# Optimization experiments

Measured on AMD Instinct MI355X. Metric: run time of the kernel, lower is better.

## Reference

```python
import jax, jax.numpy as jnp
import numpy as np

N = 50000
E = 800000
IN = 128
H = 128
C = 64
BN_EPS = 1e-5


def gcn_conv(x, W, b, src, dst, n_nodes):
    # GCNConv: add self-loops, symmetric normalization D^-1/2 (A+I) D^-1/2, linear, bias
    deg = jax.ops.segment_sum(jnp.ones_like(dst, dtype=x.dtype), dst, num_segments=n_nodes)
    dinv = jnp.where(deg > 0, jax.lax.rsqrt(deg), jnp.zeros_like(deg))
    norm = dinv[src] * dinv[dst]                      # [E+N]
    h = x @ W                                         # [N, out]
    agg = jax.ops.segment_sum(norm[:, None] * h[src], dst, num_segments=n_nodes)
    return agg + b


def batch_norm_eval(x, gamma, beta, mean, var):
    return gamma * (x - mean) * jax.lax.rsqrt(var + BN_EPS) + beta


def setup_inputs() -> dict:
    key = jax.random.key(0)
    ks = jax.random.split(key, 16)
    inp = {
        "x": jax.random.normal(ks[0], (N, IN), dtype=jnp.float32),
        "edge_index": jax.random.randint(ks[1], (2, E), 0, N, dtype=jnp.int64),
        "W1": jax.random.normal(ks[2], (IN, H), dtype=jnp.float32) / np.sqrt(IN),
        "b1": jnp.zeros((H,), dtype=jnp.float32),
        "g1": jnp.ones((H,), dtype=jnp.float32),
        "be1": jnp.zeros((H,), dtype=jnp.float32),
        "m1": jax.random.normal(ks[3], (H,), dtype=jnp.float32) * 0.1,
        "v1": jax.random.uniform(ks[4], (H,), dtype=jnp.float32, minval=0.5, maxval=1.5),
        "W2": jax.random.normal(ks[5], (H, H), dtype=jnp.float32) / np.sqrt(H),
        "b2": jnp.zeros((H,), dtype=jnp.float32),
        "g2": jnp.ones((H,), dtype=jnp.float32),
        "be2": jnp.zeros((H,), dtype=jnp.float32),
        "m2": jax.random.normal(ks[6], (H,), dtype=jnp.float32) * 0.1,
        "v2": jax.random.uniform(ks[7], (H,), dtype=jnp.float32, minval=0.5, maxval=1.5),
        "W3": jax.random.normal(ks[8], (H, C), dtype=jnp.float32) / np.sqrt(H),
        "b3": jnp.zeros((C,), dtype=jnp.float32),
    }
    return inp


def reference(x, edge_index, W1, b1, g1, be1, m1, v1, W2, b2, g2, be2, m2, v2, W3, b3):
    # add self loops once (shared across layers, GCNConv cached=True)
    loop = jnp.arange(N, dtype=edge_index.dtype)
    src = jnp.concatenate([edge_index[0], loop])
    dst = jnp.concatenate([edge_index[1], loop])

    h = gcn_conv(x, W1, b1, src, dst, N)
    h = jax.nn.relu(batch_norm_eval(h, g1, be1, m1, v1))  # eval mode: dropout is identity
    h = gcn_conv(h, W2, b2, src, dst, N)
    h = jax.nn.relu(batch_norm_eval(h, g2, be2, m2, v2))
    out = gcn_conv(h, W3, b3, src, dst, N)
    return out
```

## Files before the change

### kernel.cpp

```cpp
#include <hip/hip_runtime.h>


#define SCAN_CHUNK 1024
#define NCHUNK 256
#define BSHIFT 8
#define BWID 256
#define ECAP 8192

typedef __attribute__((ext_vector_type(8))) short bf16x8;
typedef __attribute__((ext_vector_type(4))) float f32x4;

__device__ __forceinline__ float blo(unsigned p) { return __uint_as_float(p << 16); }
__device__ __forceinline__ float bhi(unsigned p) { return __uint_as_float(p & 0xffff0000u); }
__device__ __forceinline__ unsigned short f2b(float f) {
  unsigned u = __float_as_uint(f);
  unsigned r = (u + 0x7fffu + ((u >> 16) & 1u)) >> 16;
  return (unsigned short)r;
}

__global__ void wprep_kernel(const float* __restrict__ W1, const float* __restrict__ W2,
                             const float* __restrict__ W3,
                             const float* __restrict__ b1, const float* __restrict__ g1,
                             const float* __restrict__ be1, const float* __restrict__ m1,
                             const float* __restrict__ v1,
                             const float* __restrict__ b2, const float* __restrict__ g2,
                             const float* __restrict__ be2, const float* __restrict__ m2,
                             const float* __restrict__ v2,
                             unsigned short* __restrict__ Wt1,
                             unsigned short* __restrict__ Wt2,
                             unsigned short* __restrict__ Wt3,
                             float* __restrict__ sc1, float* __restrict__ sh1,
                             float* __restrict__ sc2, float* __restrict__ sh2) {
  int i = blockIdx.x * 256 + threadIdx.x;
  if (i < 16384) {
    int k = i >> 7, c = i & 127;
    Wt1[c * 128 + k] = f2b(W1[i]);
  } else if (i < 32768) {
    int j = i - 16384; int k = j >> 7, c = j & 127;
    Wt2[c * 128 + k] = f2b(W2[j]);
  } else if (i < 40960) {
    int j = i - 32768; int k = j >> 6, c = j & 63;
    Wt3[c * 128 + k] = f2b(W3[j]);
  } else if (i < 41088) {
    int c = i - 40960;
    float s = g1[c] * rsqrtf(v1[c] + 1e-5f);
    sc1[c] = s; sh1[c] = (b1[c] - m1[c]) * s + be1[c];
  } else if (i < 41216) {
    int c = i - 41088;
    float s = g2[c] * rsqrtf(v2[c] + 1e-5f);
    sc2[c] = s; sh2[c] = (b2[c] - m2[c]) * s + be2[c];
  }
}

__global__ __launch_bounds__(256) void bin_hist_kernel(
    const int* __restrict__ ei32, const long long* __restrict__ ei64,
    int* __restrict__ counts, int E, int nbk) {
  __shared__ int hist[BWID];
  __shared__ int s_is32;
  int k = blockIdx.x, t = threadIdx.x;
  hist[t] = 0;
  if (t == 0) s_is32 = 0;
  int CH = (E + NCHUNK - 1) / NCHUNK;
  int e0 = k * CH, e1 = min(e0 + CH, E);
  __syncthreads();
  if (t < 64 && e0 + t < E && ei32[2 * (e0 + t) + 1] != 0) atomicOr(&s_is32, 1);
  __syncthreads();
  int is32 = s_is32;
  for (int e = e0 + t; e < e1; e += 256) {
    int d = is32 ? ei32[E + e] : (int)ei64[E + e];
    atomicAdd(&hist[d >> BSHIFT], 1);
  }
  __syncthreads();
  if (t < nbk) counts[t * NCHUNK + k] = hist[t];
}

__global__ __launch_bounds__(256) void scan_partial_kernel(
    const int* __restrict__ src, int* __restrict__ bsum, int n) {
  __shared__ int wsum[4];
  int b = blockIdx.x, t = threadIdx.x;
  int lane = t & 63, wv = t >> 6;
  int i0 = b * SCAN_CHUNK + t * 4;
  int4 d4 = make_int4(0, 0, 0, 0);
  if (i0 + 3 < n) d4 = *(const int4*)&src[i0];
  else {
    if (i0 < n) d4.x = src[i0];
    if (i0 + 1 < n) d4.y = src[i0 + 1];
    if (i0 + 2 < n) d4.z = src[i0 + 2];
  }
  int s = d4.x + d4.y + d4.z + d4.w;
#pragma unroll
  for (int off = 32; off; off >>= 1) s += __shfl_xor(s, off);
  if (lane == 0) wsum[wv] = s;
  __syncthreads();
  if (t == 0) bsum[b] = wsum[0] + wsum[1] + wsum[2] + wsum[3];
}

template <bool DEG>
__global__ __launch_bounds__(256) void scan_write_kernel(
    const int* __restrict__ src, const int* __restrict__ bsum,
    int* __restrict__ outp, float* __restrict__ dinv, int n, int nb) {
  __shared__ int woff[4];
  __shared__ int s_boff;
  int b = blockIdx.x, t = threadIdx.x;
  int lane = t & 63, wv = t >> 6;
  if (t < 64) {
    int v = (t < nb) ? bsum[t] : 0;
    int ic = v;
#pragma unroll
    for (int off = 1; off < 64; off <<= 1) {
      int u = __shfl_up(ic, off);
      if (t >= off) ic += u;
    }
    if (t == b) s_boff = ic - v;
    if (b == nb - 1 && t == 63) outp[n] = ic;
  }
  int i0 = b * SCAN_CHUNK + t * 4;
  int4 d4 = make_int4(0, 0, 0, 0);
  if (i0 + 3 < n) d4 = *(const int4*)&src[i0];
  else {
    if (i0 < n) d4.x = src[i0];
    if (i0 + 1 < n) d4.y = src[i0 + 1];
    if (i0 + 2 < n) d4.z = src[i0 + 2];
  }
  int tsum = d4.x + d4.y + d4.z + d4.w;
  int inc = tsum;
#pragma unroll
  for (int off = 1; off < 64; off <<= 1) {
    int u = __shfl_up(inc, off);
    if (lane >= off) inc += u;
  }
  if (lane == 63) woff[wv] = inc;
  __syncthreads();
  if (t == 0) {
    int r = 0;
#pragma unroll
    for (int w = 0; w < 4; ++w) { int sw = woff[w]; woff[w] = r; r += sw; }
  }
  __syncthreads();
  int p = inc - tsum + woff[wv] + s_boff;
  int dg[4] = {d4.x, d4.y, d4.z, d4.w};
#pragma unroll
  for (int j = 0; j < 4; ++j) {
    int i = i0 + j;
    if (i < n) {
      outp[i] = p;
      if constexpr (DEG) dinv[i] = rsqrtf((float)(dg[j] + 1));
      p += dg[j];
    }
  }
}

__global__ __launch_bounds__(256) void bin_scatter_kernel(
    const int* __restrict__ ei32, const long long* __restrict__ ei64,
    const int* __restrict__ offs, unsigned* __restrict__ pairs, int E, int nbk) {
  __shared__ int cur[BWID];
  __shared__ int s_is32;
  int k = blockIdx.x, t = threadIdx.x;
  if (t < nbk) cur[t] = offs[t * NCHUNK + k];
  if (t == 0) s_is32 = 0;
  int CH = (E + NCHUNK - 1) / NCHUNK;
  int e0 = k * CH, e1 = min(e0 + CH, E);
  __syncthreads();
  if (t < 64 && e0 + t < E && ei32[2 * (e0 + t) + 1] != 0) atomicOr(&s_is32, 1);
  __syncthreads();
  int is32 = s_is32;
  for (int e = e0 + t; e < e1; e += 256) {
    int s, d;
    if (is32) { s = ei32[e]; d = ei32[E + e]; }
    else      { s = (int)ei64[e]; d = (int)ei64[E + e]; }
    int pos = atomicAdd(&cur[d >> BSHIFT], 1);
    pairs[pos] = (unsigned)s | ((unsigned)(d & (BWID - 1)) << 20);
  }
}

__global__ __launch_bounds__(256) void bucket_deg_kernel(
    const unsigned* __restrict__ pairs, const int* __restrict__ offs,
    int* __restrict__ degi, int E, int n, int nbk) {
  __shared__ int deg[BWID];
  int b = blockIdx.x, t = threadIdx.x;
  deg[t] = 0;
  __syncthreads();
  int base = offs[b * NCHUNK];
  int end = (b + 1 < nbk) ? offs[(b + 1) * NCHUNK] : E;
  for (int i = base + t; i < end; i += 256) {
    atomicAdd(&deg[pairs[i] >> 20], 1);
  }
  __syncthreads();
  int idx = b * BWID + t;
  if (idx < n) degi[idx] = deg[t];
}

__global__ __launch_bounds__(256) void bucket_col_kernel(
    const unsigned* __restrict__ pairs, const int* __restrict__ offs,
    const int* __restrict__ rowptr, const float* __restrict__ dinv,
    uint2* __restrict__ cw, int E, int n, int nbk) {
  __shared__ int cur[BWID];
  __shared__ float dsl[BWID];
  __shared__ int stage_s[ECAP];
  __shared__ float stage_w[ECAP];
  int b = blockIdx.x, t = threadIdx.x;
  int rowbase = rowptr[b * BWID];
  int idx = b * BWID + t;
  cur[t] = ((idx < n) ? rowptr[idx] : rowptr[n]) - rowbase;
  dsl[t] = (idx < n) ? dinv[idx] : 0.f;
  __syncthreads();
  int base = offs[b * NCHUNK];
  int end = (b + 1 < nbk) ? offs[(b + 1) * NCHUNK] : E;
  for (int i = base + t; i < end; i += 256) {
    unsigned p = pairs[i];
    int s = (int)(p & 0xFFFFFu);
    int dl = (int)(p >> 20);
    int pos = atomicAdd(&cur[dl], 1);
    if (pos < ECAP) { stage_s[pos] = s; stage_w[pos] = dinv[s] * dsl[dl]; }
  }
  __syncthreads();
  int hi = b * BWID + BWID;
  int nE = ((hi < n) ? rowptr[hi] : rowptr[n]) - rowbase;
  for (int i = t; i < nE; i += 256)
    cw[rowbase + i] = make_uint2((unsigned)stage_s[i], __float_as_uint(stage_w[i]));
}

template <int HOUT, int ABF16>
__global__ __launch_bounds__(256) void mgemm_kernel(
    const void* __restrict__ Ain, const unsigned short* __restrict__ Wt,
    unsigned short* __restrict__ Y, int n) {
  constexpr int NT = HOUT;
  __shared__ unsigned char AsB[64 * 256];
  __shared__ unsigned char BsB[NT * 256];
  int t = threadIdx.x;
  int row0 = blockIdx.x * 64;

  if constexpr (ABF16) {
    const unsigned short* A = (const unsigned short*)Ain;
#pragma unroll
    for (int jj = 0; jj < 4; ++jj) {
      int f = t + 256 * jj; int r = f >> 4, kq = f & 15;
      uint4 v = make_uint4(0, 0, 0, 0);
      if (row0 + r < n) v = *(const uint4*)&A[(size_t)(row0 + r) * 128 + kq * 8];
      *(uint4*)&AsB[r * 256 + ((kq * 16) ^ ((r & 15) << 4))] = v;
    }
  } else {
    const float* A = (const float*)Ain;
#pragma unroll
    for (int jj = 0; jj < 8; ++jj) {
      int f = t + 256 * jj; int r = f >> 5, kq = f & 31;
      float4 v = make_float4(0.f, 0.f, 0.f, 0.f);
      if (row0 + r < n) v = *(const float4*)&A[(size_t)(row0 + r) * 128 + kq * 4];
      unsigned two0 = (unsigned)f2b(v.x) | ((unsigned)f2b(v.y) << 16);
      unsigned two1 = (unsigned)f2b(v.z) | ((unsigned)f2b(v.w) << 16);
      uint2 o = make_uint2(two0, two1);
      *(uint2*)&AsB[r * 256 + ((kq * 8) ^ ((r & 15) << 4))] = o;
    }
  }
#pragma unroll
  for (int jj = 0; jj < NT / 16; ++jj) {
    int f = t + 256 * jj; int c = f >> 4, kq = f & 15;
    uint4 v = *(const uint4*)&Wt[(size_t)c * 128 + kq * 8];
    *(uint4*)&BsB[c * 256 + ((kq * 16) ^ ((c & 15) << 4))] = v;
  }
  __syncthreads();

  int l = t & 63, wid = t >> 6;
  constexpr int WC = NT / 2;
  constexpr int NI = WC / 16;
  int wr = (wid >> 1) * 32, wc = (wid & 1) * WC;
  int lr = l & 15, lk = (l >> 4) * 16;

  f32x4 acc[2][NI] = {};
#pragma unroll
  for (int ks = 0; ks < 4; ++ks) {
    bf16x8 a[2], b[NI];
#pragma unroll
    for (int mi = 0; mi < 2; ++mi) {
      int r = wr + mi * 16 + lr;
      a[mi] = *(const bf16x8*)&AsB[r * 256 + ((ks * 64 + lk) ^ ((r & 15) << 4))];
    }
#pragma unroll
    for (int ni = 0; ni < NI; ++ni) {
      int c = wc + ni * 16 + lr;
      b[ni] = *(const bf16x8*)&BsB[c * 256 + ((ks * 64 + lk) ^ ((c & 15) << 4))];
    }
#pragma unroll
    for (int mi = 0; mi < 2; ++mi)
#pragma unroll
      for (int ni = 0; ni < NI; ++ni)
        acc[mi][ni] = __builtin_amdgcn_mfma_f32_16x16x32_bf16(a[mi], b[ni],
                                                              acc[mi][ni], 0, 0, 0);
  }

#pragma unroll
  for (int mi = 0; mi < 2; ++mi) {
#pragma unroll
    for (int reg = 0; reg < 4; ++reg) {
      int gr = row0 + wr + mi * 16 + (l >> 4) * 4 + reg;
      if (gr < n) {
#pragma unroll
        for (int ni = 0; ni < NI; ++ni) {
          int gc = wc + ni * 16 + lr;
          Y[(size_t)gr * HOUT + gc] = f2b(acc[mi][ni][reg]);
        }
      }
    }
  }
}

template <int HOUT, bool BN, bool OUTBF>
__global__ __launch_bounds__(256) void agg_kernel(
    const unsigned short* __restrict__ h, const int* __restrict__ rowptr,
    const uint2* __restrict__ cw, const float* __restrict__ dinv,
    const float* __restrict__ sc, const float* __restrict__ sh,
    void* __restrict__ out, int n_nodes) {
  int n = (blockIdx.x * blockDim.x + threadIdx.x) >> 6;
  if (n >= n_nodes) return;
  int lane = threadIdx.x & 63;
  const uint2* hu2 = (const uint2*)h;
  constexpr int RW2 = HOUT / 4;
  constexpr int NPH = (HOUT == 128) ? 2 : 4;
  constexpr int GL = 64 / NPH;
  int phase = lane / GL;
  int sub = lane & (GL - 1);

  float dn = dinv[n];
  int beg = rowptr[n], end = rowptr[n + 1];
  float a0 = 0.f, a1 = 0.f, a2 = 0.f, a3 = 0.f;
  if (phase == 0) {
    uint2 sp = hu2[(size_t)n * RW2 + sub];
    float sw = dn * dn;
    a0 = sw * blo(sp.x); a1 = sw * bhi(sp.x);
    a2 = sw * blo(sp.y); a3 = sw * bhi(sp.y);
  }

  int j = beg + phase;
  for (; j + 3 * NPH < end; j += 4 * NPH) {
    uint2 e0 = cw[j], e1 = cw[j + NPH], e2 = cw[j + 2 * NPH], e3 = cw[j + 3 * NPH];
    uint2 h0 = hu2[(size_t)e0.x * RW2 + sub];
    uint2 h1 = hu2[(size_t)e1.x * RW2 + sub];
    uint2 h2 = hu2[(size_t)e2.x * RW2 + sub];
    uint2 h3 = hu2[(size_t)e3.x * RW2 + sub];
    float w0 = __uint_as_float(e0.y), w1 = __uint_as_float(e1.y);
    float w2 = __uint_as_float(e2.y), w3 = __uint_as_float(e3.y);
    a0 = fmaf(w0, blo(h0.x), a0); a1 = fmaf(w0, bhi(h0.x), a1);
    a2 = fmaf(w0, blo(h0.y), a2); a3 = fmaf(w0, bhi(h0.y), a3);
    a0 = fmaf(w1, blo(h1.x), a0); a1 = fmaf(w1, bhi(h1.x), a1);
    a2 = fmaf(w1, blo(h1.y), a2); a3 = fmaf(w1, bhi(h1.y), a3);
    a0 = fmaf(w2, blo(h2.x), a0); a1 = fmaf(w2, bhi(h2.x), a1);
    a2 = fmaf(w2, blo(h2.y), a2); a3 = fmaf(w2, bhi(h2.y), a3);
    a0 = fmaf(w3, blo(h3.x), a0); a1 = fmaf(w3, bhi(h3.x), a1);
    a2 = fmaf(w3, blo(h3.y), a2); a3 = fmaf(w3, bhi(h3.y), a3);
  }
  for (; j < end; j += NPH) {
    uint2 e = cw[j];
    uint2 hv = hu2[(size_t)e.x * RW2 + sub];
    float w = __uint_as_float(e.y);
    a0 = fmaf(w, blo(hv.x), a0); a1 = fmaf(w, bhi(hv.x), a1);
    a2 = fmaf(w, blo(hv.y), a2); a3 = fmaf(w, bhi(hv.y), a3);
  }

  a0 += __shfl_xor(a0, 32); a1 += __shfl_xor(a1, 32);
  a2 += __shfl_xor(a2, 32); a3 += __shfl_xor(a3, 32);
  if constexpr (NPH == 4) {
    a0 += __shfl_xor(a0, 16); a1 += __shfl_xor(a1, 16);
    a2 += __shfl_xor(a2, 16); a3 += __shfl_xor(a3, 16);
  }
  if (phase != 0) return;

  int c0 = sub * 4;
  float y0, y1, y2, y3;
  if constexpr (BN) {
    y0 = fmaxf(fmaf(a0, sc[c0], sh[c0]), 0.f);
    y1 = fmaxf(fmaf(a1, sc[c0 + 1], sh[c0 + 1]), 0.f);
    y2 = fmaxf(fmaf(a2, sc[c0 + 2], sh[c0 + 2]), 0.f);
    y3 = fmaxf(fmaf(a3, sc[c0 + 3], sh[c0 + 3]), 0.f);
  } else {
    y0 = a0 + sh[c0]; y1 = a1 + sh[c0 + 1];
    y2 = a2 + sh[c0 + 2]; y3 = a3 + sh[c0 + 3];
  }
  if constexpr (OUTBF) {
    unsigned p0 = (unsigned)f2b(y0) | ((unsigned)f2b(y1) << 16);
    unsigned p1 = (unsigned)f2b(y2) | ((unsigned)f2b(y3) << 16);
    ((uint2*)out)[(size_t)n * RW2 + sub] = make_uint2(p0, p1);
  } else {
    float4 o; o.x = y0; o.y = y1; o.z = y2; o.w = y3;
    *(float4*)&((float*)out)[(size_t)n * HOUT + c0] = o;
  }
}

extern "C" void kernel_launch(void* const* d_in, const int* in_sizes, int n_in,
                              void* d_out, int out_size, void* d_ws, size_t ws_size,
                              hipStream_t stream) {
  const float* x = (const float*)d_in[0];
  const int* ei32 = (const int*)d_in[1];
  const long long* ei64 = (const long long*)d_in[1];
  const float* W1 = (const float*)d_in[2];
  const float* b1 = (const float*)d_in[3];
  const float* g1 = (const float*)d_in[4];
  const float* be1 = (const float*)d_in[5];
  const float* m1 = (const float*)d_in[6];
  const float* v1 = (const float*)d_in[7];
  const float* W2 = (const float*)d_in[8];
  const float* b2 = (const float*)d_in[9];
  const float* g2 = (const float*)d_in[10];
  const float* be2 = (const float*)d_in[11];
  const float* m2 = (const float*)d_in[12];
  const float* v2 = (const float*)d_in[13];
  const float* W3 = (const float*)d_in[14];
  const float* b3 = (const float*)d_in[15];

  const int N = in_sizes[0] / 128;
  const int E = in_sizes[1] / 2;
  const int NBK = (N + BWID - 1) / BWID;
  const int NC = NBK * NCHUNK;

  char* ws = (char*)d_ws;
  size_t off = 0;
  auto alloc = [&](size_t bytes) -> void* {
    void* p = ws + off;
    off = (off + bytes + 255) & ~(size_t)255;
    return p;
  };
  float* dinv = (float*)alloc((size_t)N * 4);
  int* rowptr = (int*)alloc((size_t)(N + 1) * 4);
  int* degi = (int*)alloc((size_t)N * 4);
  int* counts = (int*)alloc((size_t)(NC + 1) * 4);
  int* offs = (int*)alloc((size_t)(NC + 1) * 4);
  uint2* cw = (uint2*)alloc((size_t)E * 8);
  unsigned* pairs = (unsigned*)alloc((size_t)E * 4);
  int* bsum = (int*)alloc(64 * 4);
  unsigned short* wt1 = (unsigned short*)alloc(128 * 128 * 2);
  unsigned short* wt2 = (unsigned short*)alloc(128 * 128 * 2);
  unsigned short* wt3 = (unsigned short*)alloc(128 * 64 * 2);
  float* sc1 = (float*)alloc(128 * 4);
  float* sh1 = (float*)alloc(128 * 4);
  float* sc2 = (float*)alloc(128 * 4);
  float* sh2 = (float*)alloc(128 * 4);
  unsigned short* hbuf = (unsigned short*)alloc((size_t)N * 128 * 2);
  unsigned short* ybuf = (unsigned short*)alloc((size_t)N * 128 * 2);
  (void)ws_size;

  wprep_kernel<<<161, 256, 0, stream>>>(W1, W2, W3, b1, g1, be1, m1, v1,
                                        b2, g2, be2, m2, v2,
                                        wt1, wt2, wt3, sc1, sh1, sc2, sh2);

  bin_hist_kernel<<<NCHUNK, 256, 0, stream>>>(ei32, ei64, counts, E, NBK);
  int nbC = (NC + SCAN_CHUNK - 1) / SCAN_CHUNK;
  scan_partial_kernel<<<nbC, 256, 0, stream>>>(counts, bsum, NC);
  scan_write_kernel<false><<<nbC, 256, 0, stream>>>(counts, bsum, offs, nullptr, NC, nbC);
  bin_scatter_kernel<<<NCHUNK, 256, 0, stream>>>(ei32, ei64, offs, pairs, E, NBK);
  bucket_deg_kernel<<<NBK, 256, 0, stream>>>(pairs, offs, degi, E, N, NBK);
  int nbN = (N + SCAN_CHUNK - 1) / SCAN_CHUNK;
  scan_partial_kernel<<<nbN, 256, 0, stream>>>(degi, bsum, N);
  scan_write_kernel<true><<<nbN, 256, 0, stream>>>(degi, bsum, rowptr, dinv, N, nbN);
  bucket_col_kernel<<<NBK, 256, 0, stream>>>(pairs, offs, rowptr, dinv, cw, E, N, NBK);

  int gb = (N + 63) / 64;
  int ab = (N + 3) / 4;

  mgemm_kernel<128, 0><<<gb, 256, 0, stream>>>(x, wt1, hbuf, N);
  agg_kernel<128, true, true><<<ab, 256, 0, stream>>>(hbuf, rowptr, cw, dinv,
                                                      sc1, sh1, ybuf, N);
  mgemm_kernel<128, 1><<<gb, 256, 0, stream>>>(ybuf, wt2, hbuf, N);
  agg_kernel<128, true, true><<<ab, 256, 0, stream>>>(hbuf, rowptr, cw, dinv,
                                                      sc2, sh2, ybuf, N);
  mgemm_kernel<64, 1><<<gb, 256, 0, stream>>>(ybuf, wt3, hbuf, N);
  agg_kernel<64, false, false><<<ab, 256, 0, stream>>>(hbuf, rowptr, cw, dinv,
                                                       nullptr, b3, d_out, N);
}
```

Baseline: 188.7 us.

## Sort edges by source slab, fold self-loops into CSR, widen aggregation loads

The binning key now combines the destination bucket with a source slab of 8192 nodes. Edges inside each row are then roughly ordered by source, which should improve cache locality of the gathers during aggregation. The degree pass computes rowptr and dinv directly from per-bucket offsets plus self-loops, which removes the separate node-level scan kernels. Self-loops are written as explicit CSR entries, so the aggregation kernel no longer handles them specially. That kernel now loads 16-byte bf16 vectors with more edges per phase. In exchange the count array is 8 times larger, there is an overflow path for rows beyond the staging capacity, and register use per lane is higher.

```diff
diff --git a/kernel.cpp b/kernel.cpp
--- a/kernel.cpp
+++ b/kernel.cpp
@@ -1,10 +1,11 @@
 #include <hip/hip_runtime.h>
 
 
-#define SCAN_CHUNK 1024
 #define NCHUNK 256
 #define BSHIFT 8
 #define BWID 256
+#define NSLAB 8
+#define SSHIFT 13
 #define ECAP 8192
 
 typedef __attribute__((ext_vector_type(8))) short bf16x8;
@@ -54,11 +55,11 @@
 
 __global__ __launch_bounds__(256) void bin_hist_kernel(
     const int* __restrict__ ei32, const long long* __restrict__ ei64,
-    int* __restrict__ counts, int E, int nbk) {
-  __shared__ int hist[BWID];
+    int* __restrict__ counts, int E, int nkeys) {
+  __shared__ int hist[2048];
   __shared__ int s_is32;
   int k = blockIdx.x, t = threadIdx.x;
-  hist[t] = 0;
+  for (int i = t; i < nkeys; i += 256) hist[i] = 0;
   if (t == 0) s_is32 = 0;
   int CH = (E + NCHUNK - 1) / NCHUNK;
   int e0 = k * CH, e1 = min(e0 + CH, E);
@@ -67,27 +68,34 @@
   __syncthreads();
   int is32 = s_is32;
   for (int e = e0 + t; e < e1; e += 256) {
-    int d = is32 ? ei32[E + e] : (int)ei64[E + e];
-    atomicAdd(&hist[d >> BSHIFT], 1);
-  }
-  __syncthreads();
-  if (t < nbk) counts[t * NCHUNK + k] = hist[t];
-}
-
+    int s, d;
+    if (is32) { s = ei32[e]; d = ei32[E + e]; }
+    else      { s = (int)ei64[e]; d = (int)ei64[E + e]; }
+    atomicAdd(&hist[((d >> BSHIFT) << 3) | (s >> SSHIFT)], 1);
+  }
+  __syncthreads();
+  for (int i = t; i < nkeys; i += 256) counts[i * NCHUNK + k] = hist[i];
+}
+
+template <int CHUNK>
 __global__ __launch_bounds__(256) void scan_partial_kernel(
     const int* __restrict__ src, int* __restrict__ bsum, int n) {
   __shared__ int wsum[4];
+  constexpr int EL = CHUNK / 256;
   int b = blockIdx.x, t = threadIdx.x;
   int lane = t & 63, wv = t >> 6;
-  int i0 = b * SCAN_CHUNK + t * 4;
-  int4 d4 = make_int4(0, 0, 0, 0);
-  if (i0 + 3 < n) d4 = *(const int4*)&src[i0];
-  else {
-    if (i0 < n) d4.x = src[i0];
-    if (i0 + 1 < n) d4.y = src[i0 + 1];
-    if (i0 + 2 < n) d4.z = src[i0 + 2];
-  }
-  int s = d4.x + d4.y + d4.z + d4.w;
+  int s = 0;
+  int i0 = b * CHUNK + t * EL;
+#pragma unroll
+  for (int q = 0; q < EL / 4; ++q) {
+    int i = i0 + q * 4;
+    if (i + 3 < n) {
+      int4 d4 = *(const int4*)&src[i];
+      s += d4.x + d4.y + d4.z + d4.w;
+    } else {
+      for (int r = 0; r < 4; ++r) if (i + r < n) s += src[i + r];
+    }
+  }
 #pragma unroll
   for (int off = 32; off; off >>= 1) s += __shfl_xor(s, off);
   if (lane == 0) wsum[wv] = s;
@@ -95,10 +103,11 @@
   if (t == 0) bsum[b] = wsum[0] + wsum[1] + wsum[2] + wsum[3];
 }
 
-template <bool DEG>
+template <int CHUNK>
 __global__ __launch_bounds__(256) void scan_write_kernel(
     const int* __restrict__ src, const int* __restrict__ bsum,
-    int* __restrict__ outp, float* __restrict__ dinv, int n, int nb) {
+    int* __restrict__ outp, int n, int nb) {
+  constexpr int EL = CHUNK / 256;
   __shared__ int woff[4];
   __shared__ int s_boff;
   int b = blockIdx.x, t = threadIdx.x;
@@ -114,15 +123,24 @@
     if (t == b) s_boff = ic - v;
     if (b == nb - 1 && t == 63) outp[n] = ic;
   }
-  int i0 = b * SCAN_CHUNK + t * 4;
-  int4 d4 = make_int4(0, 0, 0, 0);
-  if (i0 + 3 < n) d4 = *(const int4*)&src[i0];
-  else {
-    if (i0 < n) d4.x = src[i0];
-    if (i0 + 1 < n) d4.y = src[i0 + 1];
-    if (i0 + 2 < n) d4.z = src[i0 + 2];
-  }
-  int tsum = d4.x + d4.y + d4.z + d4.w;
+  int vals[EL];
+  int i0 = b * CHUNK + t * EL;
+#pragma unroll
+  for (int q = 0; q < EL / 4; ++q) {
+    int i = i0 + q * 4;
+    int4 d4 = make_int4(0, 0, 0, 0);
+    if (i + 3 < n) d4 = *(const int4*)&src[i];
+    else {
+      if (i < n) d4.x = src[i];
+      if (i + 1 < n) d4.y = src[i + 1];
+      if (i + 2 < n) d4.z = src[i + 2];
+    }
+    vals[q * 4] = d4.x; vals[q * 4 + 1] = d4.y;
+    vals[q * 4 + 2] = d4.z; vals[q * 4 + 3] = d4.w;
+  }
+  int tsum = 0;
+#pragma unroll
+  for (int q = 0; q < EL; ++q) tsum += vals[q];
   int inc = tsum;
 #pragma unroll
   for (int off = 1; off < 64; off <<= 1) {
@@ -138,25 +156,21 @@
   }
   __syncthreads();
   int p = inc - tsum + woff[wv] + s_boff;
-  int dg[4] = {d4.x, d4.y, d4.z, d4.w};
-#pragma unroll
-  for (int j = 0; j < 4; ++j) {
-    int i = i0 + j;
-    if (i < n) {
-      outp[i] = p;
-      if constexpr (DEG) dinv[i] = rsqrtf((float)(dg[j] + 1));
-      p += dg[j];
-    }
+#pragma unroll
+  for (int q = 0; q < EL; ++q) {
+    int i = i0 + q;
+    if (i < n) outp[i] = p;
+    p += vals[q];
   }
 }
 
 __global__ __launch_bounds__(256) void bin_scatter_kernel(
     const int* __restrict__ ei32, const long long* __restrict__ ei64,
-    const int* __restrict__ offs, unsigned* __restrict__ pairs, int E, int nbk) {
-  __shared__ int cur[BWID];
+    const int* __restrict__ offs, unsigned* __restrict__ pairs, int E, int nkeys) {
+  __shared__ int cur[2048];
   __shared__ int s_is32;
   int k = blockIdx.x, t = threadIdx.x;
-  if (t < nbk) cur[t] = offs[t * NCHUNK + k];
+  for (int i = t; i < nkeys; i += 256) cur[i] = offs[i * NCHUNK + k];
   if (t == 0) s_is32 = 0;
   int CH = (E + NCHUNK - 1) / NCHUNK;
   int e0 = k * CH, e1 = min(e0 + CH, E);
@@ -168,56 +182,88 @@
     int s, d;
     if (is32) { s = ei32[e]; d = ei32[E + e]; }
     else      { s = (int)ei64[e]; d = (int)ei64[E + e]; }
-    int pos = atomicAdd(&cur[d >> BSHIFT], 1);
+    int pos = atomicAdd(&cur[((d >> BSHIFT) << 3) | (s >> SSHIFT)], 1);
     pairs[pos] = (unsigned)s | ((unsigned)(d & (BWID - 1)) << 20);
   }
 }
 
-__global__ __launch_bounds__(256) void bucket_deg_kernel(
+__global__ __launch_bounds__(256) void bucket_p1_kernel(
     const unsigned* __restrict__ pairs, const int* __restrict__ offs,
-    int* __restrict__ degi, int E, int n, int nbk) {
+    int* __restrict__ rowptr, float* __restrict__ dinv, int E, int n) {
   __shared__ int deg[BWID];
+  __shared__ int woff[4];
   int b = blockIdx.x, t = threadIdx.x;
+  int lane = t & 63, wv = t >> 6;
   deg[t] = 0;
   __syncthreads();
-  int base = offs[b * NCHUNK];
-  int end = (b + 1 < nbk) ? offs[(b + 1) * NCHUNK] : E;
-  for (int i = base + t; i < end; i += 256) {
+  int basep = offs[b * NSLAB * NCHUNK];
+  int endp = offs[(b + 1) * NSLAB * NCHUNK];
+  for (int i = basep + t; i < endp; i += 256)
     atomicAdd(&deg[pairs[i] >> 20], 1);
-  }
-  __syncthreads();
+  __syncthreads();
+  int dg = deg[t];
+  int inc = dg + 1;
+#pragma unroll
+  for (int off = 1; off < 64; off <<= 1) {
+    int u = __shfl_up(inc, off);
+    if (lane >= off) inc += u;
+  }
+  if (lane == 63) woff[wv] = inc;
+  __syncthreads();
+  if (t == 0) {
+    int r = 0;
+#pragma unroll
+    for (int w = 0; w < 4; ++w) { int sw = woff[w]; woff[w] = r; r += sw; }
+  }
+  __syncthreads();
+  int exc = inc - (dg + 1) + woff[wv];
+  int cwbase = basep + b * BWID;
   int idx = b * BWID + t;
-  if (idx < n) degi[idx] = deg[t];
-}
-
-__global__ __launch_bounds__(256) void bucket_col_kernel(
+  if (idx < n) {
+    rowptr[idx] = cwbase + exc;
+    dinv[idx] = rsqrtf((float)(dg + 1));
+  }
+  if (b == 0 && t == 0) rowptr[n] = E + n;
+}
+
+__global__ __launch_bounds__(256) void bucket_p2_kernel(
     const unsigned* __restrict__ pairs, const int* __restrict__ offs,
     const int* __restrict__ rowptr, const float* __restrict__ dinv,
-    uint2* __restrict__ cw, int E, int n, int nbk) {
+    uint2* __restrict__ cw, int E, int n) {
   __shared__ int cur[BWID];
   __shared__ float dsl[BWID];
   __shared__ int stage_s[ECAP];
   __shared__ float stage_w[ECAP];
   int b = blockIdx.x, t = threadIdx.x;
-  int rowbase = rowptr[b * BWID];
+  int basep = offs[b * NSLAB * NCHUNK];
+  int endp = offs[(b + 1) * NSLAB * NCHUNK];
+  int cwbase = basep + b * BWID;
   int idx = b * BWID + t;
-  cur[t] = ((idx < n) ? rowptr[idx] : rowptr[n]) - rowbase;
-  dsl[t] = (idx < n) ? dinv[idx] : 0.f;
-  __syncthreads();
-  int base = offs[b * NCHUNK];
-  int end = (b + 1 < nbk) ? offs[(b + 1) * NCHUNK] : E;
-  for (int i = base + t; i < end; i += 256) {
+  int nreal = min(n - b * BWID, BWID);
+  float dv = (t < nreal) ? dinv[idx] : 0.f;
+  dsl[t] = dv;
+  cur[t] = (t < nreal) ? rowptr[idx] - cwbase : 0;
+  __syncthreads();
+  if (t < nreal) {
+    int pos = atomicAdd(&cur[t], 1);
+    if (pos < ECAP) { stage_s[pos] = idx; stage_w[pos] = dv * dv; }
+    else cw[cwbase + pos] = make_uint2((unsigned)idx, __float_as_uint(dv * dv));
+  }
+  __syncthreads();
+  for (int i = basep + t; i < endp; i += 256) {
     unsigned p = pairs[i];
     int s = (int)(p & 0xFFFFFu);
     int dl = (int)(p >> 20);
     int pos = atomicAdd(&cur[dl], 1);
-    if (pos < ECAP) { stage_s[pos] = s; stage_w[pos] = dinv[s] * dsl[dl]; }
-  }
-  __syncthreads();
-  int hi = b * BWID + BWID;
-  int nE = ((hi < n) ? rowptr[hi] : rowptr[n]) - rowbase;
-  for (int i = t; i < nE; i += 256)
-    cw[rowbase + i] = make_uint2((unsigned)stage_s[i], __float_as_uint(stage_w[i]));
+    float w = dinv[s] * dsl[dl];
+    if (pos < ECAP) { stage_s[pos] = s; stage_w[pos] = w; }
+    else cw[cwbase + pos] = make_uint2((unsigned)s, __float_as_uint(w));
+  }
+  __syncthreads();
+  int nE = (endp - basep) + nreal;
+  int lim = min(nE, ECAP);
+  for (int i = t; i < lim; i += 256)
+    cw[cwbase + i] = make_uint2((unsigned)stage_s[i], __float_as_uint(stage_w[i]));
 }
 
 template <int HOUT, int ABF16>
@@ -307,81 +353,85 @@
 template <int HOUT, bool BN, bool OUTBF>
 __global__ __launch_bounds__(256) void agg_kernel(
     const unsigned short* __restrict__ h, const int* __restrict__ rowptr,
-    const uint2* __restrict__ cw, const float* __restrict__ dinv,
+    const uint2* __restrict__ cw,
     const float* __restrict__ sc, const float* __restrict__ sh,
     void* __restrict__ out, int n_nodes) {
   int n = (blockIdx.x * blockDim.x + threadIdx.x) >> 6;
   if (n >= n_nodes) return;
   int lane = threadIdx.x & 63;
-  const uint2* hu2 = (const uint2*)h;
-  constexpr int RW2 = HOUT / 4;
-  constexpr int NPH = (HOUT == 128) ? 2 : 4;
-  constexpr int GL = 64 / NPH;
+  constexpr int GL = HOUT / 8;
+  constexpr int NPH = 64 / GL;
   int phase = lane / GL;
   int sub = lane & (GL - 1);
-
-  float dn = dinv[n];
+  const uint4* hu = (const uint4*)h;
+
   int beg = rowptr[n], end = rowptr[n + 1];
-  float a0 = 0.f, a1 = 0.f, a2 = 0.f, a3 = 0.f;
-  if (phase == 0) {
-    uint2 sp = hu2[(size_t)n * RW2 + sub];
-    float sw = dn * dn;
-    a0 = sw * blo(sp.x); a1 = sw * bhi(sp.x);
-    a2 = sw * blo(sp.y); a3 = sw * bhi(sp.y);
-  }
+  float a[8] = {0.f, 0.f, 0.f, 0.f, 0.f, 0.f, 0.f, 0.f};
 
   int j = beg + phase;
   for (; j + 3 * NPH < end; j += 4 * NPH) {
     uint2 e0 = cw[j], e1 = cw[j + NPH], e2 = cw[j + 2 * NPH], e3 = cw[j + 3 * NPH];
-    uint2 h0 = hu2[(size_t)e0.x * RW2 + sub];
-    uint2 h1 = hu2[(size_t)e1.x * RW2 + sub];
-    uint2 h2 = hu2[(size_t)e2.x * RW2 + sub];
-    uint2 h3 = hu2[(size_t)e3.x * RW2 + sub];
+    uint4 h0 = hu[(size_t)e0.x * GL + sub];
+    uint4 h1 = hu[(size_t)e1.x * GL + sub];
+    uint4 h2 = hu[(size_t)e2.x * GL + sub];
+    uint4 h3 = hu[(size_t)e3.x * GL + sub];
     float w0 = __uint_as_float(e0.y), w1 = __uint_as_float(e1.y);
     float w2 = __uint_as_float(e2.y), w3 = __uint_as_float(e3.y);
-    a0 = fmaf(w0, blo(h0.x), a0); a1 = fmaf(w0, bhi(h0.x), a1);
-    a2 = fmaf(w0, blo(h0.y), a2); a3 = fmaf(w0, bhi(h0.y), a3);
-    a0 = fmaf(w1, blo(h1.x), a0); a1 = fmaf(w1, bhi(h1.x), a1);
-    a2 = fmaf(w1, blo(h1.y), a2); a3 = fmaf(w1, bhi(h1.y), a3);
-    a0 = fmaf(w2, blo(h2.x), a0); a1 = fmaf(w2, bhi(h2.x), a1);
-    a2 = fmaf(w2, blo(h2.y), a2); a3 = fmaf(w2, bhi(h2.y), a3);
-    a0 = fmaf(w3, blo(h3.x), a0); a1 = fmaf(w3, bhi(h3.x), a1);
-    a2 = fmaf(w3, blo(h3.y), a2); a3 = fmaf(w3, bhi(h3.y), a3);
+    a[0] = fmaf(w0, blo(h0.x), a[0]); a[1] = fmaf(w0, bhi(h0.x), a[1]);
+    a[2] = fmaf(w0, blo(h0.y), a[2]); a[3] = fmaf(w0, bhi(h0.y), a[3]);
+    a[4] = fmaf(w0, blo(h0.z), a[4]); a[5] = fmaf(w0, bhi(h0.z), a[5]);
+    a[6] = fmaf(w0, blo(h0.w), a[6]); a[7] = fmaf(w0, bhi(h0.w), a[7]);
+    a[0] = fmaf(w1, blo(h1.x), a[0]); a[1] = fmaf(w1, bhi(h1.x), a[1]);
+    a[2] = fmaf(w1, blo(h1.y), a[2]); a[3] = fmaf(w1, bhi(h1.y), a[3]);
+    a[4] = fmaf(w1, blo(h1.z), a[4]); a[5] = fmaf(w1, bhi(h1.z), a[5]);
+    a[6] = fmaf(w1, blo(h1.w), a[6]); a[7] = fmaf(w1, bhi(h1.w), a[7]);
+    a[0] = fmaf(w2, blo(h2.x), a[0]); a[1] = fmaf(w2, bhi(h2.x), a[1]);
+    a[2] = fmaf(w2, blo(h2.y), a[2]); a[3] = fmaf(w2, bhi(h2.y), a[3]);
+    a[4] = fmaf(w2, blo(h2.z), a[4]); a[5] = fmaf(w2, bhi(h2.z), a[5]);
+    a[6] = fmaf(w2, blo(h2.w), a[6]); a[7] = fmaf(w2, bhi(h2.w), a[7]);
+    a[0] = fmaf(w3, blo(h3.x), a[0]); a[1] = fmaf(w3, bhi(h3.x), a[1]);
+    a[2] = fmaf(w3, blo(h3.y), a[2]); a[3] = fmaf(w3, bhi(h3.y), a[3]);
+    a[4] = fmaf(w3, blo(h3.z), a[4]); a[5] = fmaf(w3, bhi(h3.z), a[5]);
+    a[6] = fmaf(w3, blo(h3.w), a[6]); a[7] = fmaf(w3, bhi(h3.w), a[7]);
   }
   for (; j < end; j += NPH) {
     uint2 e = cw[j];
-    uint2 hv = hu2[(size_t)e.x * RW2 + sub];
+    uint4 hv = hu[(size_t)e.x * GL + sub];
     float w = __uint_as_float(e.y);
-    a0 = fmaf(w, blo(hv.x), a0); a1 = fmaf(w, bhi(hv.x), a1);
-    a2 = fmaf(w, blo(hv.y), a2); a3 = fmaf(w, bhi(hv.y), a3);
-  }
-
-  a0 += __shfl_xor(a0, 32); a1 += __shfl_xor(a1, 32);
-  a2 += __shfl_xor(a2, 32); a3 += __shfl_xor(a3, 32);
-  if constexpr (NPH == 4) {
-    a0 += __shfl_xor(a0, 16); a1 += __shfl_xor(a1, 16);
-    a2 += __shfl_xor(a2, 16); a3 += __shfl_xor(a3, 16);
+    a[0] = fmaf(w, blo(hv.x), a[0]); a[1] = fmaf(w, bhi(hv.x), a[1]);
+    a[2] = fmaf(w, blo(hv.y), a[2]); a[3] = fmaf(w, bhi(hv.y), a[3]);
+    a[4] = fmaf(w, blo(hv.z), a[4]); a[5] = fmaf(w, bhi(hv.z), a[5]);
+    a[6] = fmaf(w, blo(hv.w), a[6]); a[7] = fmaf(w, bhi(hv.w), a[7]);
+  }
+
+#pragma unroll
+  for (int q = 0; q < 8; ++q) {
+    a[q] += __shfl_xor(a[q], 32);
+    a[q] += __shfl_xor(a[q], 16);
+    if constexpr (NPH == 8) a[q] += __shfl_xor(a[q], 8);
   }
   if (phase != 0) return;
 
-  int c0 = sub * 4;
-  float y0, y1, y2, y3;
-  if constexpr (BN) {
-    y0 = fmaxf(fmaf(a0, sc[c0], sh[c0]), 0.f);
-    y1 = fmaxf(fmaf(a1, sc[c0 + 1], sh[c0 + 1]), 0.f);
-    y2 = fmaxf(fmaf(a2, sc[c0 + 2], sh[c0 + 2]), 0.f);
-    y3 = fmaxf(fmaf(a3, sc[c0 + 3], sh[c0 + 3]), 0.f);
+  int c0 = sub * 8;
+  float y[8];
+#pragma unroll
+  for (int q = 0; q < 8; ++q) {
+    if constexpr (BN) y[q] = fmaxf(fmaf(a[q], sc[c0 + q], sh[c0 + q]), 0.f);
+    else y[q] = a[q] + sh[c0 + q];
+  }
+  if constexpr (OUTBF) {
+    uint4 o;
+    o.x = (unsigned)f2b(y[0]) | ((unsigned)f2b(y[1]) << 16);
+    o.y = (unsigned)f2b(y[2]) | ((unsigned)f2b(y[3]) << 16);
+    o.z = (unsigned)f2b(y[4]) | ((unsigned)f2b(y[5]) << 16);
+    o.w = (unsigned)f2b(y[6]) | ((unsigned)f2b(y[7]) << 16);
+    ((uint4*)out)[(size_t)n * GL + sub] = o;
   } else {
-    y0 = a0 + sh[c0]; y1 = a1 + sh[c0 + 1];
-    y2 = a2 + sh[c0 + 2]; y3 = a3 + sh[c0 + 3];
-  }
-  if constexpr (OUTBF) {
-    unsigned p0 = (unsigned)f2b(y0) | ((unsigned)f2b(y1) << 16);
-    unsigned p1 = (unsigned)f2b(y2) | ((unsigned)f2b(y3) << 16);
-    ((uint2*)out)[(size_t)n * RW2 + sub] = make_uint2(p0, p1);
-  } else {
-    float4 o; o.x = y0; o.y = y1; o.z = y2; o.w = y3;
-    *(float4*)&((float*)out)[(size_t)n * HOUT + c0] = o;
+    float* op = (float*)out + (size_t)n * HOUT + c0;
+    float4 o0; o0.x = y[0]; o0.y = y[1]; o0.z = y[2]; o0.w = y[3];
+    float4 o1; o1.x = y[4]; o1.y = y[5]; o1.z = y[6]; o1.w = y[7];
+    *(float4*)op = o0;
+    *(float4*)(op + 4) = o1;
   }
 }
 
@@ -409,7 +459,8 @@
   const int N = in_sizes[0] / 128;
   const int E = in_sizes[1] / 2;
   const int NBK = (N + BWID - 1) / BWID;
-  const int NC = NBK * NCHUNK;
+  const int NKEYS = NBK * NSLAB;
+  const int NC = NKEYS * NCHUNK;
 
   char* ws = (char*)d_ws;
   size_t off = 0;
@@ -420,11 +471,10 @@
   };
   float* dinv = (float*)alloc((size_t)N * 4);
   int* rowptr = (int*)alloc((size_t)(N + 1) * 4);
-  int* degi = (int*)alloc((size_t)N * 4);
-  int* counts = (int*)alloc((size_t)(NC + 1) * 4);
+  int* counts = (int*)alloc((size_t)NC * 4);
   int* offs = (int*)alloc((size_t)(NC + 1) * 4);
-  uint2* cw = (uint2*)alloc((size_t)E * 8);
   unsigned* pairs = (unsigned*)alloc((size_t)E * 4);
+  uint2* cw = (uint2*)alloc((size_t)(E + N) * 8);
   int* bsum = (int*)alloc(64 * 4);
   unsigned short* wt1 = (unsigned short*)alloc(128 * 128 * 2);
   unsigned short* wt2 = (unsigned short*)alloc(128 * 128 * 2);
@@ -441,27 +491,24 @@
                                         b2, g2, be2, m2, v2,
                                         wt1, wt2, wt3, sc1, sh1, sc2, sh2);
 
-  bin_hist_kernel<<<NCHUNK, 256, 0, stream>>>(ei32, ei64, counts, E, NBK);
-  int nbC = (NC + SCAN_CHUNK - 1) / SCAN_CHUNK;
-  scan_partial_kernel<<<nbC, 256, 0, stream>>>(counts, bsum, NC);
-  scan_write_kernel<false><<<nbC, 256, 0, stream>>>(counts, bsum, offs, nullptr, NC, nbC);
-  bin_scatter_kernel<<<NCHUNK, 256, 0, stream>>>(ei32, ei64, offs, pairs, E, NBK);
-  bucket_deg_kernel<<<NBK, 256, 0, stream>>>(pairs, offs, degi, E, N, NBK);
-  int nbN = (N + SCAN_CHUNK - 1) / SCAN_CHUNK;
-  scan_partial_kernel<<<nbN, 256, 0, stream>>>(degi, bsum, N);
-  scan_write_kernel<true><<<nbN, 256, 0, stream>>>(degi, bsum, rowptr, dinv, N, nbN);
-  bucket_col_kernel<<<NBK, 256, 0, stream>>>(pairs, offs, rowptr, dinv, cw, E, N, NBK);
+  bin_hist_kernel<<<NCHUNK, 256, 0, stream>>>(ei32, ei64, counts, E, NKEYS);
+  int nbC = (NC + 8191) / 8192;
+  scan_partial_kernel<8192><<<nbC, 256, 0, stream>>>(counts, bsum, NC);
+  scan_write_kernel<8192><<<nbC, 256, 0, stream>>>(counts, bsum, offs, NC, nbC);
+  bin_scatter_kernel<<<NCHUNK, 256, 0, stream>>>(ei32, ei64, offs, pairs, E, NKEYS);
+  bucket_p1_kernel<<<NBK, 256, 0, stream>>>(pairs, offs, rowptr, dinv, E, N);
+  bucket_p2_kernel<<<NBK, 256, 0, stream>>>(pairs, offs, rowptr, dinv, cw, E, N);
 
   int gb = (N + 63) / 64;
   int ab = (N + 3) / 4;
 
   mgemm_kernel<128, 0><<<gb, 256, 0, stream>>>(x, wt1, hbuf, N);
-  agg_kernel<128, true, true><<<ab, 256, 0, stream>>>(hbuf, rowptr, cw, dinv,
+  agg_kernel<128, true, true><<<ab, 256, 0, stream>>>(hbuf, rowptr, cw,
                                                       sc1, sh1, ybuf, N);
   mgemm_kernel<128, 1><<<gb, 256, 0, stream>>>(ybuf, wt2, hbuf, N);
-  agg_kernel<128, true, true><<<ab, 256, 0, stream>>>(hbuf, rowptr, cw, dinv,
+  agg_kernel<128, true, true><<<ab, 256, 0, stream>>>(hbuf, rowptr, cw,
                                                       sc2, sh2, ybuf, N);
   mgemm_kernel<64, 1><<<gb, 256, 0, stream>>>(ybuf, wt3, hbuf, N);
-  agg_kernel<64, false, false><<<ab, 256, 0, stream>>>(hbuf, rowptr, cw, dinv,
+  agg_kernel<64, false, false><<<ab, 256, 0, stream>>>(hbuf, rowptr, cw,
                                                        nullptr, b3, d_out, N);
 }
```

Measured after the change: 184.0 us. 1.03x faster.

## Merge CSR build kernels and compute edge weights on the fly in aggregation

Applied to the files above, without the earlier changes.

Folds weight preparation into the histogram kernel and merges degree counting, row-pointer scan and column placement into one per-bucket kernel that scans within the bucket. The CSR now stores only source indices, and the aggregation kernels compute the normalization weight from dinv at the destination and source. This removes several kernel launches and an intermediate buffer, and halves the edge-list bytes read in each layer. In exchange it adds a random gather of dinv per edge.

```diff
diff --git a/kernel.cpp b/kernel.cpp
--- a/kernel.cpp
+++ b/kernel.cpp
@@ -18,46 +18,46 @@
   return (unsigned short)r;
 }
 
-__global__ void wprep_kernel(const float* __restrict__ W1, const float* __restrict__ W2,
-                             const float* __restrict__ W3,
-                             const float* __restrict__ b1, const float* __restrict__ g1,
-                             const float* __restrict__ be1, const float* __restrict__ m1,
-                             const float* __restrict__ v1,
-                             const float* __restrict__ b2, const float* __restrict__ g2,
-                             const float* __restrict__ be2, const float* __restrict__ m2,
-                             const float* __restrict__ v2,
-                             unsigned short* __restrict__ Wt1,
-                             unsigned short* __restrict__ Wt2,
-                             unsigned short* __restrict__ Wt3,
-                             float* __restrict__ sc1, float* __restrict__ sh1,
-                             float* __restrict__ sc2, float* __restrict__ sh2) {
-  int i = blockIdx.x * 256 + threadIdx.x;
-  if (i < 16384) {
-    int k = i >> 7, c = i & 127;
-    Wt1[c * 128 + k] = f2b(W1[i]);
-  } else if (i < 32768) {
-    int j = i - 16384; int k = j >> 7, c = j & 127;
-    Wt2[c * 128 + k] = f2b(W2[j]);
-  } else if (i < 40960) {
-    int j = i - 32768; int k = j >> 6, c = j & 63;
-    Wt3[c * 128 + k] = f2b(W3[j]);
-  } else if (i < 41088) {
-    int c = i - 40960;
-    float s = g1[c] * rsqrtf(v1[c] + 1e-5f);
-    sc1[c] = s; sh1[c] = (b1[c] - m1[c]) * s + be1[c];
-  } else if (i < 41216) {
-    int c = i - 41088;
-    float s = g2[c] * rsqrtf(v2[c] + 1e-5f);
-    sc2[c] = s; sh2[c] = (b2[c] - m2[c]) * s + be2[c];
-  }
-}
-
-__global__ __launch_bounds__(256) void bin_hist_kernel(
+__global__ __launch_bounds__(256) void histprep_kernel(
     const int* __restrict__ ei32, const long long* __restrict__ ei64,
-    int* __restrict__ counts, int E, int nbk) {
+    int* __restrict__ counts, int E, int nbk,
+    const float* __restrict__ W1, const float* __restrict__ W2,
+    const float* __restrict__ W3,
+    const float* __restrict__ b1, const float* __restrict__ g1,
+    const float* __restrict__ be1, const float* __restrict__ m1,
+    const float* __restrict__ v1,
+    const float* __restrict__ b2, const float* __restrict__ g2,
+    const float* __restrict__ be2, const float* __restrict__ m2,
+    const float* __restrict__ v2,
+    unsigned short* __restrict__ Wt1, unsigned short* __restrict__ Wt2,
+    unsigned short* __restrict__ Wt3,
+    float* __restrict__ sc1, float* __restrict__ sh1,
+    float* __restrict__ sc2, float* __restrict__ sh2) {
   __shared__ int hist[BWID];
   __shared__ int s_is32;
   int k = blockIdx.x, t = threadIdx.x;
+  if (k >= NCHUNK) {
+    int i = (k - NCHUNK) * 256 + t;
+    if (i < 16384) {
+      int kk = i >> 7, c = i & 127;
+      Wt1[c * 128 + kk] = f2b(W1[i]);
+    } else if (i < 32768) {
+      int j = i - 16384; int kk = j >> 7, c = j & 127;
+      Wt2[c * 128 + kk] = f2b(W2[j]);
+    } else if (i < 40960) {
+      int j = i - 32768; int kk = j >> 6, c = j & 63;
+      Wt3[c * 128 + kk] = f2b(W3[j]);
+    } else if (i < 41088) {
+      int c = i - 40960;
+      float s = g1[c] * rsqrtf(v1[c] + 1e-5f);
+      sc1[c] = s; sh1[c] = (b1[c] - m1[c]) * s + be1[c];
+    } else if (i < 41216) {
+      int c = i - 41088;
+      float s = g2[c] * rsqrtf(v2[c] + 1e-5f);
+      sc2[c] = s; sh2[c] = (b2[c] - m2[c]) * s + be2[c];
+    }
+    return;
+  }
   hist[t] = 0;
   if (t == 0) s_is32 = 0;
   int CH = (E + NCHUNK - 1) / NCHUNK;
@@ -95,10 +95,9 @@
   if (t == 0) bsum[b] = wsum[0] + wsum[1] + wsum[2] + wsum[3];
 }
 
-template <bool DEG>
 __global__ __launch_bounds__(256) void scan_write_kernel(
     const int* __restrict__ src, const int* __restrict__ bsum,
-    int* __restrict__ outp, float* __restrict__ dinv, int n, int nb) {
+    int* __restrict__ outp, int n, int nb) {
   __shared__ int woff[4];
   __shared__ int s_boff;
   int b = blockIdx.x, t = threadIdx.x;
@@ -142,11 +141,8 @@
 #pragma unroll
   for (int j = 0; j < 4; ++j) {
     int i = i0 + j;
-    if (i < n) {
-      outp[i] = p;
-      if constexpr (DEG) dinv[i] = rsqrtf((float)(dg[j] + 1));
-      p += dg[j];
-    }
+    if (i < n) outp[i] = p;
+    p += dg[j];
   }
 }
 
@@ -173,51 +169,59 @@
   }
 }
 
-__global__ __launch_bounds__(256) void bucket_deg_kernel(
+__global__ __launch_bounds__(256) void bucket_merged_kernel(
     const unsigned* __restrict__ pairs, const int* __restrict__ offs,
-    int* __restrict__ degi, int E, int n, int nbk) {
+    int* __restrict__ rowptr, float* __restrict__ dinv,
+    int* __restrict__ col, int E, int n, int nbk) {
   __shared__ int deg[BWID];
+  __shared__ int cur[BWID];
+  __shared__ int woff[4];
+  __shared__ int stage_s[ECAP];
   int b = blockIdx.x, t = threadIdx.x;
+  int lane = t & 63, wv = t >> 6;
   deg[t] = 0;
   __syncthreads();
-  int base = offs[b * NCHUNK];
-  int end = (b + 1 < nbk) ? offs[(b + 1) * NCHUNK] : E;
-  for (int i = base + t; i < end; i += 256) {
+  int basep = offs[b * NCHUNK];
+  int endp = (b + 1 < nbk) ? offs[(b + 1) * NCHUNK] : E;
+  for (int i = basep + t; i < endp; i += 256)
     atomicAdd(&deg[pairs[i] >> 20], 1);
-  }
-  __syncthreads();
+  __syncthreads();
+  int dg = deg[t];
+  int inc = dg;
+#pragma unroll
+  for (int off = 1; off < 64; off <<= 1) {
+    int u = __shfl_up(inc, off);
+    if (lane >= off) inc += u;
+  }
+  if (lane == 63) woff[wv] = inc;
+  __syncthreads();
+  if (t == 0) {
+    int r = 0;
+#pragma unroll
+    for (int w = 0; w < 4; ++w) { int sw = woff[w]; woff[w] = r; r += sw; }
+  }
+  __syncthreads();
+  int exc = inc - dg + woff[wv];
   int idx = b * BWID + t;
-  if (idx < n) degi[idx] = deg[t];
-}
-
-__global__ __launch_bounds__(256) void bucket_col_kernel(
-    const unsigned* __restrict__ pairs, const int* __restrict__ offs,
-    const int* __restrict__ rowptr, const float* __restrict__ dinv,
-    uint2* __restrict__ cw, int E, int n, int nbk) {
-  __shared__ int cur[BWID];
-  __shared__ float dsl[BWID];
-  __shared__ int stage_s[ECAP];
-  __shared__ float stage_w[ECAP];
-  int b = blockIdx.x, t = threadIdx.x;
-  int rowbase = rowptr[b * BWID];
-  int idx = b * BWID + t;
-  cur[t] = ((idx < n) ? rowptr[idx] : rowptr[n]) - rowbase;
-  dsl[t] = (idx < n) ? dinv[idx] : 0.f;
-  __syncthreads();
-  int base = offs[b * NCHUNK];
-  int end = (b + 1 < nbk) ? offs[(b + 1) * NCHUNK] : E;
-  for (int i = base + t; i < end; i += 256) {
+  if (idx < n) {
+    rowptr[idx] = basep + exc;
+    dinv[idx] = rsqrtf((float)(dg + 1));
+  }
+  cur[t] = exc;
+  __syncthreads();
+  for (int i = basep + t; i < endp; i += 256) {
     unsigned p = pairs[i];
     int s = (int)(p & 0xFFFFFu);
     int dl = (int)(p >> 20);
     int pos = atomicAdd(&cur[dl], 1);
-    if (pos < ECAP) { stage_s[pos] = s; stage_w[pos] = dinv[s] * dsl[dl]; }
-  }
-  __syncthreads();
-  int hi = b * BWID + BWID;
-  int nE = ((hi < n) ? rowptr[hi] : rowptr[n]) - rowbase;
-  for (int i = t; i < nE; i += 256)
-    cw[rowbase + i] = make_uint2((unsigned)stage_s[i], __float_as_uint(stage_w[i]));
+    if (pos < ECAP) stage_s[pos] = s;
+    else col[basep + pos] = s;
+  }
+  __syncthreads();
+  int nE = endp - basep;
+  int lim = min(nE, ECAP);
+  for (int i = t; i < lim; i += 256) col[basep + i] = stage_s[i];
+  if (b == 0 && t == 0) rowptr[n] = E;
 }
 
 template <int HOUT, int ABF16>
@@ -307,7 +311,7 @@
 template <int HOUT, bool BN, bool OUTBF>
 __global__ __launch_bounds__(256) void agg_kernel(
     const unsigned short* __restrict__ h, const int* __restrict__ rowptr,
-    const uint2* __restrict__ cw, const float* __restrict__ dinv,
+    const int* __restrict__ col, const float* __restrict__ dinv,
     const float* __restrict__ sc, const float* __restrict__ sh,
     void* __restrict__ out, int n_nodes) {
   int n = (blockIdx.x * blockDim.x + threadIdx.x) >> 6;
@@ -332,13 +336,14 @@
 
   int j = beg + phase;
   for (; j + 3 * NPH < end; j += 4 * NPH) {
-    uint2 e0 = cw[j], e1 = cw[j + NPH], e2 = cw[j + 2 * NPH], e3 = cw[j + 3 * NPH];
-    uint2 h0 = hu2[(size_t)e0.x * RW2 + sub];
-    uint2 h1 = hu2[(size_t)e1.x * RW2 + sub];
-    uint2 h2 = hu2[(size_t)e2.x * RW2 + sub];
-    uint2 h3 = hu2[(size_t)e3.x * RW2 + sub];
-    float w0 = __uint_as_float(e0.y), w1 = __uint_as_float(e1.y);
-    float w2 = __uint_as_float(e2.y), w3 = __uint_as_float(e3.y);
+    int s0 = col[j],           s1 = col[j + NPH];
+    int s2 = col[j + 2 * NPH], s3 = col[j + 3 * NPH];
+    uint2 h0 = hu2[(size_t)s0 * RW2 + sub];
+    uint2 h1 = hu2[(size_t)s1 * RW2 + sub];
+    uint2 h2 = hu2[(size_t)s2 * RW2 + sub];
+    uint2 h3 = hu2[(size_t)s3 * RW2 + sub];
+    float w0 = dn * dinv[s0], w1 = dn * dinv[s1];
+    float w2 = dn * dinv[s2], w3 = dn * dinv[s3];
     a0 = fmaf(w0, blo(h0.x), a0); a1 = fmaf(w0, bhi(h0.x), a1);
     a2 = fmaf(w0, blo(h0.y), a2); a3 = fmaf(w0, bhi(h0.y), a3);
     a0 = fmaf(w1, blo(h1.x), a0); a1 = fmaf(w1, bhi(h1.x), a1);
@@ -349,9 +354,9 @@
     a2 = fmaf(w3, blo(h3.y), a2); a3 = fmaf(w3, bhi(h3.y), a3);
   }
   for (; j < end; j += NPH) {
-    uint2 e = cw[j];
-    uint2 hv = hu2[(size_t)e.x * RW2 + sub];
-    float w = __uint_as_float(e.y);
+    int s = col[j];
+    uint2 hv = hu2[(size_t)s * RW2 + sub];
+    float w = dn * dinv[s];
     a0 = fmaf(w, blo(hv.x), a0); a1 = fmaf(w, bhi(hv.x), a1);
     a2 = fmaf(w, blo(hv.y), a2); a3 = fmaf(w, bhi(hv.y), a3);
   }
@@ -420,10 +425,9 @@
   };
   float* dinv = (float*)alloc((size_t)N * 4);
   int* rowptr = (int*)alloc((size_t)(N + 1) * 4);
-  int* degi = (int*)alloc((size_t)N * 4);
   int* counts = (int*)alloc((size_t)(NC + 1) * 4);
   int* offs = (int*)alloc((size_t)(NC + 1) * 4);
-  uint2* cw = (uint2*)alloc((size_t)E * 8);
+  int* col = (int*)alloc((size_t)E * 4);
   unsigned* pairs = (unsigned*)alloc((size_t)E * 4);
   int* bsum = (int*)alloc(64 * 4);
   unsigned short* wt1 = (unsigned short*)alloc(128 * 128 * 2);
@@ -437,31 +441,27 @@
   unsigned short* ybuf = (unsigned short*)alloc((size_t)N * 128 * 2);
   (void)ws_size;
 
-  wprep_kernel<<<161, 256, 0, stream>>>(W1, W2, W3, b1, g1, be1, m1, v1,
-                                        b2, g2, be2, m2, v2,
-                                        wt1, wt2, wt3, sc1, sh1, sc2, sh2);
-
-  bin_hist_kernel<<<NCHUNK, 256, 0, stream>>>(ei32, ei64, counts, E, NBK);
+  histprep_kernel<<<NCHUNK + 161, 256, 0, stream>>>(
+      ei32, ei64, counts, E, NBK,
+      W1, W2, W3, b1, g1, be1, m1, v1, b2, g2, be2, m2, v2,
+      wt1, wt2, wt3, sc1, sh1, sc2, sh2);
   int nbC = (NC + SCAN_CHUNK - 1) / SCAN_CHUNK;
   scan_partial_kernel<<<nbC, 256, 0, stream>>>(counts, bsum, NC);
-  scan_write_kernel<false><<<nbC, 256, 0, stream>>>(counts, bsum, offs, nullptr, NC, nbC);
+  scan_write_kernel<<<nbC, 256, 0, stream>>>(counts, bsum, offs, NC, nbC);
   bin_scatter_kernel<<<NCHUNK, 256, 0, stream>>>(ei32, ei64, offs, pairs, E, NBK);
-  bucket_deg_kernel<<<NBK, 256, 0, stream>>>(pairs, offs, degi, E, N, NBK);
-  int nbN = (N + SCAN_CHUNK - 1) / SCAN_CHUNK;
-  scan_partial_kernel<<<nbN, 256, 0, stream>>>(degi, bsum, N);
-  scan_write_kernel<true><<<nbN, 256, 0, stream>>>(degi, bsum, rowptr, dinv, N, nbN);
-  bucket_col_kernel<<<NBK, 256, 0, stream>>>(pairs, offs, rowptr, dinv, cw, E, N, NBK);
+  bucket_merged_kernel<<<NBK, 256, 0, stream>>>(pairs, offs, rowptr, dinv,
+                                                col, E, N, NBK);
 
   int gb = (N + 63) / 64;
   int ab = (N + 3) / 4;
 
   mgemm_kernel<128, 0><<<gb, 256, 0, stream>>>(x, wt1, hbuf, N);
-  agg_kernel<128, true, true><<<ab, 256, 0, stream>>>(hbuf, rowptr, cw, dinv,
+  agg_kernel<128, true, true><<<ab, 256, 0, stream>>>(hbuf, rowptr, col, dinv,
                                                       sc1, sh1, ybuf, N);
   mgemm_kernel<128, 1><<<gb, 256, 0, stream>>>(ybuf, wt2, hbuf, N);
-  agg_kernel<128, true, true><<<ab, 256, 0, stream>>>(hbuf, rowptr, cw, dinv,
+  agg_kernel<128, true, true><<<ab, 256, 0, stream>>>(hbuf, rowptr, col, dinv,
                                                       sc2, sh2, ybuf, N);
   mgemm_kernel<64, 1><<<gb, 256, 0, stream>>>(ybuf, wt3, hbuf, N);
-  agg_kernel<64, false, false><<<ab, 256, 0, stream>>>(hbuf, rowptr, cw, dinv,
+  agg_kernel<64, false, false><<<ab, 256, 0, stream>>>(hbuf, rowptr, col, dinv,
                                                        nullptr, b3, d_out, N);
 }
```

Result: faster. 165.5 us, median of 2 (-12.3%).
